# Optimization experiments

Measured on AMD Instinct MI355X. Metric: run time of the kernel, lower is better.

Reference implementation:

```python
import jax, jax.numpy as jnp
import numpy as np

NUM_HEAD = 8
GN_GROUPS = 32
EPS = 1e-5


def group_norm(x, w, b):
    # x: [B,C,H,W]; GroupNorm over 32 groups
    B, C, H, W = x.shape
    xg = x.reshape(B, GN_GROUPS, C // GN_GROUPS, H, W)
    mu = jnp.mean(xg, axis=(2, 3, 4), keepdims=True)
    var = jnp.var(xg, axis=(2, 3, 4), keepdims=True)
    xn = ((xg - mu) * jax.lax.rsqrt(var + EPS)).reshape(B, C, H, W)
    return xn * w[None, :, None, None] + b[None, :, None, None]


def conv1x1(x, w, b):
    # 1x1 conv == channel-wise linear: w [O,C], x [B,C,H,W]
    return jnp.einsum('oc,bchw->bohw', w, x) + b[None, :, None, None]


def setup_inputs() -> dict:
    key = jax.random.key(0)
    ks = jax.random.split(key, 6)
    B, C, H, W = 8, 512, 32, 32
    s = 1.0 / np.sqrt(C)
    return {
        'x': jax.random.normal(ks[0], (B, C, H, W), jnp.float32),
        'gn_w': jnp.ones((C,), jnp.float32),
        'gn_b': jnp.zeros((C,), jnp.float32),
        'wq': jax.random.normal(ks[1], (C, C), jnp.float32) * s,
        'bq': jnp.zeros((C,), jnp.float32),
        'wk': jax.random.normal(ks[2], (C, C), jnp.float32) * s,
        'bk': jnp.zeros((C,), jnp.float32),
        'wv': jax.random.normal(ks[3], (C, C), jnp.float32) * s,
        'bv': jnp.zeros((C,), jnp.float32),
        'wo': jax.random.normal(ks[4], (C, C), jnp.float32) * s,
        'bo': jnp.zeros((C,), jnp.float32),
    }


def reference(x, gn_w, gn_b, wq, bq, wk, bk, wv, bv, wo, bo):
    B, C, H, W = x.shape
    Hn = NUM_HEAD
    d = C // Hn
    N = H * W
    scale = d ** -0.5

    xn = group_norm(x, gn_w, gn_b)
    q = conv1x1(xn, wq, bq).reshape(B, Hn, d, N)  # [B,Hn,d,N]
    k = conv1x1(xn, wk, bk).reshape(B, Hn, d, N)
    v = conv1x1(xn, wv, bv).reshape(B, Hn, d, N)

    # attn[b,h,i,j] = sum_d q[b,h,d,i] * k[b,h,d,j]
    attn = jnp.einsum('bhdi,bhdj->bhij', q, k) * scale
    attn = jax.nn.softmax(attn, axis=-1)
    # out[b,h,d,i] = sum_j attn[b,h,i,j] * v[b,h,d,j]
    out = jnp.einsum('bhij,bhdj->bhdi', attn, v).reshape(B, C, H, W)
    return x + conv1x1(out, wo, bo)
```

## Files before the change

### kernel.cpp

```cpp
#include <hip/hip_runtime.h>
#include <hip/hip_bf16.h>

typedef unsigned short ushort_t;
typedef __bf16 bf16_t;
typedef bf16_t bf16x8 __attribute__((ext_vector_type(8)));
typedef float f32x4 __attribute__((ext_vector_type(4)));
typedef float f32x16 __attribute__((ext_vector_type(16)));

#define CH 512
#define NSP 1024

__device__ __forceinline__ float bf2f(ushort_t u) {
    union { unsigned int i; float f; } t; t.i = ((unsigned int)u) << 16; return t.f;
}
__device__ __forceinline__ ushort_t f2bf(float f) {
    union { float fl; unsigned int i; } t; t.fl = f;
    unsigned int r = t.i + 0x7fffu + ((t.i >> 16) & 1u);
    return (ushort_t)(r >> 16);
}
__device__ __forceinline__ unsigned int pk2(float a, float b) {
    __hip_bfloat162 h = __float22bfloat162_rn(make_float2(a, b));
    union { __hip_bfloat162 h2; unsigned int u; } t; t.h2 = h; return t.u;
}

#if __has_builtin(__builtin_amdgcn_global_load_lds)
#define HAVE_ASYNC_LDS 1
#endif
__device__ __forceinline__ void cp16(const ushort_t* g, ushort_t* l) {
#ifdef HAVE_ASYNC_LDS
    __builtin_amdgcn_global_load_lds((const __attribute__((address_space(1))) unsigned int*)g,
                                     (__attribute__((address_space(3))) unsigned int*)l, 16, 0, 0);
#else
    *(uint4*)l = *(const uint4*)g;
#endif
}

#if __has_builtin(__builtin_amdgcn_exp2f)
#define EXP2(x) __builtin_amdgcn_exp2f(x)
#else
#define EXP2(x) exp2f(x)
#endif

#define QSCALE 0.18033688011112042f

__global__ __launch_bounds__(256) void prep_kernel(const float* __restrict__ x,
                                                   const float* __restrict__ w0, const float* __restrict__ w1,
                                                   const float* __restrict__ w2, const float* __restrict__ w3,
                                                   float2* __restrict__ gstats, ushort_t* __restrict__ wbf) {
    int tid = threadIdx.x;
    if (blockIdx.x >= 256) {
        int idx = (blockIdx.x - 256) * 256 + tid;
        int my = idx >> 16;
        const float* src = (my == 0) ? w0 : (my == 1) ? w1 : (my == 2) ? w2 : w3;
        float4 v = reinterpret_cast<const float4*>(src)[idx & 65535];
        uint2 u = make_uint2(pk2(v.x, v.y), pk2(v.z, v.w));
        reinterpret_cast<uint2*>(wbf + (size_t)my * 262144)[idx & 65535] = u;
        return;
    }
    __shared__ float red[8];
    int bg = blockIdx.x;
    size_t base = (size_t)bg * 16384;
    float s = 0.f, s2 = 0.f;
    const float4* x4 = reinterpret_cast<const float4*>(x + base);
    for (int i = tid; i < 4096; i += 256) {
        float4 v = x4[i];
        s  += v.x + v.y + v.z + v.w;
        s2 += v.x * v.x + v.y * v.y + v.z * v.z + v.w * v.w;
    }
    #pragma unroll
    for (int off = 32; off > 0; off >>= 1) {
        s  += __shfl_down(s, off, 64);
        s2 += __shfl_down(s2, off, 64);
    }
    int wv = tid >> 6;
    if ((tid & 63) == 0) { red[wv] = s; red[4 + wv] = s2; }
    __syncthreads();
    if (tid == 0) {
        float ts  = red[0] + red[1] + red[2] + red[3];
        float ts2 = red[4] + red[5] + red[6] + red[7];
        float mu  = ts * (1.f / 16384.f);
        float var = ts2 * (1.f / 16384.f) - mu * mu;
        gstats[bg] = make_float2(mu, rsqrtf(var + 1e-5f));
    }
}

__global__ __launch_bounds__(256) void gn_apply(const float* __restrict__ x, const float* __restrict__ gw,
                                                const float* __restrict__ gbias, const float2* __restrict__ gstats,
                                                ushort_t* __restrict__ xnt) {
    __shared__ __align__(16) ushort_t lt[16 * 264];
    int nq = blockIdx.x;
    int bg = blockIdx.y;
    int b = bg >> 5, g = bg & 31;
    int tid = threadIdx.x;
    float2 st = gstats[bg];
    float mu = st.x, rstd = st.y;
    const float4* x4 = reinterpret_cast<const float4*>(x + ((size_t)(b * 512 + g * 16) * 1024 + nq * 256));
    #pragma unroll
    for (int rep = 0; rep < 4; rep++) {
        int id = rep * 256 + tid;
        int cc = id >> 6, j = id & 63;
        float ww = gw[g * 16 + cc], bb = gbias[g * 16 + cc];
        float ca = rstd * ww, cb = bb - mu * ca;
        float4 v = x4[cc * 256 + j];
        uint2 u = make_uint2(pk2(v.x * ca + cb, v.y * ca + cb), pk2(v.z * ca + cb, v.w * ca + cb));
        *reinterpret_cast<uint2*>(&lt[cc * 264 + j * 4]) = u;
    }
    __syncthreads();
    int n = tid;
    ushort_t ov[16];
    #pragma unroll
    for (int cc = 0; cc < 16; cc++) ov[cc] = lt[cc * 264 + n];
    ushort_t* dst = xnt + ((size_t)(b * 1024 + nq * 256 + n)) * 512 + g * 16;
    *reinterpret_cast<ushort4*>(dst + 0)  = *reinterpret_cast<ushort4*>(&ov[0]);
    *reinterpret_cast<ushort4*>(dst + 4)  = *reinterpret_cast<ushort4*>(&ov[4]);
    *reinterpret_cast<ushort4*>(dst + 8)  = *reinterpret_cast<ushort4*>(&ov[8]);
    *reinterpret_cast<ushort4*>(dst + 12) = *reinterpret_cast<ushort4*>(&ov[12]);
}

__global__ __launch_bounds__(256) void conv_qkv(const ushort_t* __restrict__ xnt,
                                                const ushort_t* __restrict__ wbf,
                                                const float* __restrict__ bq,
                                                const float* __restrict__ bk,
                                                const float* __restrict__ bv,
                                                ushort_t* __restrict__ qt,
                                                ushort_t* __restrict__ kt,
                                                ushort_t* __restrict__ vt) {
    __shared__ __align__(16) char smem[17408];
    ushort_t* als = (ushort_t*)smem;
    ushort_t* bls = (ushort_t*)(smem + 8192);
    int tid = threadIdx.x;
    int wave = tid >> 6, lane = tid & 63, l15 = lane & 15, quad = lane >> 4;
    int wm = wave >> 1, wn = wave & 1;
    int m0 = blockIdx.x * 128, o0 = blockIdx.y * 64, b = blockIdx.z;
    const ushort_t* A = xnt + (size_t)b * 524288;

    f32x4 acc[4][2];
    #pragma unroll
    for (int ms = 0; ms < 4; ms++)
        #pragma unroll
        for (int ns = 0; ns < 2; ns++) acc[ms][ns] = (f32x4){0.f, 0.f, 0.f, 0.f};

    for (int k0 = 0; k0 < 512; k0 += 32) {
        #pragma unroll
        for (int rep = 0; rep < 2; rep++) {
            int id = rep * 256 + tid;
            int r = id >> 2, part = id & 3;
            int sw = part ^ ((r >> 2) & 3);
            cp16(A + (size_t)(m0 + r) * 512 + k0 + sw * 8, als + (size_t)id * 8);
        }
        {
            int r = tid >> 2, part = tid & 3;
            int sw = part ^ ((r >> 2) & 3);
            cp16(wbf + (size_t)(o0 + r) * 512 + k0 + sw * 8, bls + (size_t)tid * 8);
        }
        __syncthreads();
        bf16x8 af[4], bfr[2];
        #pragma unroll
        for (int ms = 0; ms < 4; ms++) {
            int row = wm * 64 + ms * 16 + l15;
            int slot = quad ^ ((row >> 2) & 3);
            af[ms] = *(const bf16x8*)(als + row * 32 + slot * 8);
        }
        #pragma unroll
        for (int ns = 0; ns < 2; ns++) {
            int row = wn * 32 + ns * 16 + l15;
            int slot = quad ^ ((row >> 2) & 3);
            bfr[ns] = *(const bf16x8*)(bls + row * 32 + slot * 8);
        }
        #pragma unroll
        for (int ms = 0; ms < 4; ms++)
            #pragma unroll
            for (int ns = 0; ns < 2; ns++)
                acc[ms][ns] = __builtin_amdgcn_mfma_f32_16x16x32_bf16(af[ms], bfr[ns], acc[ms][ns], 0, 0, 0);
        __syncthreads();
    }

    int seg = o0 >> 9, lo = o0 & 511;
    if (seg < 2) {
        const float* bias = seg ? bk : bq;
        ushort_t* dst = seg ? kt : qt;
        float s = seg ? 1.f : QSCALE;
        float bv0 = bias[lo + wn * 32 + l15];
        float bv1 = bias[lo + wn * 32 + 16 + l15];
        ushort_t* cls = (ushort_t*)smem;
        #pragma unroll
        for (int ms = 0; ms < 4; ms++)
            #pragma unroll
            for (int ns = 0; ns < 2; ns++) {
                float bb = ns ? bv1 : bv0;
                int idx = (wm * 64 + ms * 16 + quad * 4) * 64 + wn * 32 + ns * 16 + l15;
                unsigned int ua = pk2((acc[ms][ns][0] + bb) * s, (acc[ms][ns][1] + bb) * s);
                unsigned int ub = pk2((acc[ms][ns][2] + bb) * s, (acc[ms][ns][3] + bb) * s);
                cls[idx]       = (ushort_t)(ua & 0xffff);
                cls[idx + 64]  = (ushort_t)(ua >> 16);
                cls[idx + 128] = (ushort_t)(ub & 0xffff);
                cls[idx + 192] = (ushort_t)(ub >> 16);
            }
        __syncthreads();
        int h = lo >> 6;
        size_t obase = ((size_t)(b * 8 + h) * 1024 + m0) * 64;
        #pragma unroll
        for (int rep = 0; rep < 4; rep++) {
            int id = rep * 256 + tid;
            int r = id >> 3, part = id & 7;
            *(uint4*)(dst + obase + (size_t)r * 64 + part * 8) = *(const uint4*)(cls + r * 64 + part * 8);
        }
    } else {
        float bv0 = bv[lo + wn * 32 + l15];
        float bv1 = bv[lo + wn * 32 + 16 + l15];
        ushort_t* clst = (ushort_t*)smem;
        #pragma unroll
        for (int ms = 0; ms < 4; ms++)
            #pragma unroll
            for (int ns = 0; ns < 2; ns++) {
                float bb = ns ? bv1 : bv0;
                unsigned int ua = pk2(acc[ms][ns][0] + bb, acc[ms][ns][1] + bb);
                unsigned int ub = pk2(acc[ms][ns][2] + bb, acc[ms][ns][3] + bb);
                *(uint2*)(&clst[(wn * 32 + ns * 16 + l15) * 136 + wm * 64 + ms * 16 + quad * 4]) =
                    make_uint2(ua, ub);
            }
        __syncthreads();
        #pragma unroll
        for (int rep = 0; rep < 4; rep++) {
            int id = rep * 256 + tid;
            int row = id >> 4, part = id & 15;
            *(uint4*)(vt + ((size_t)(b * 512 + lo + row) * 1024 + m0 + part * 8)) =
                *(const uint4*)(clst + row * 136 + part * 8);
        }
    }
}

#define Z16 {0.f,0.f,0.f,0.f,0.f,0.f,0.f,0.f,0.f,0.f,0.f,0.f,0.f,0.f,0.f,0.f}

#define PV_STEP(JS, P) {                                                                     \
    unsigned wA0 = pk2(P[((JS)&1)*8+0], P[((JS)&1)*8+1]);                                    \
    unsigned wA1 = pk2(P[((JS)&1)*8+2], P[((JS)&1)*8+3]);                                    \
    unsigned wB0 = pk2(P[((JS)&1)*8+4], P[((JS)&1)*8+5]);                                    \
    unsigned wB1 = pk2(P[((JS)&1)*8+6], P[((JS)&1)*8+7]);                                    \
    asm("v_permlane32_swap_b32 %0, %1" : "+v"(wA0), "+v"(wB0));                              \
    asm("v_permlane32_swap_b32 %0, %1" : "+v"(wA1), "+v"(wB1));                              \
    union { unsigned u[4]; bf16x8 v; } pa_;                                                  \
    pa_.u[0] = wA0; pa_.u[1] = wA1; pa_.u[2] = wB0; pa_.u[3] = wB1;                          \
    int phys_ = (((JS) * 2) | hi) ^ r7;                                                      \
    bf16x8 vf0 = *(const bf16x8*)(vbuf + l31 * 64 + phys_ * 8);                              \
    bf16x8 vf1 = *(const bf16x8*)(vbuf + (32 + l31) * 64 + phys_ * 8);                       \
    __builtin_amdgcn_s_setprio(1);                                                           \
    vacc0 = __builtin_amdgcn_mfma_f32_32x32x16_bf16(pa_.v, vf0, vacc0, 0, 0, 0);             \
    vacc1 = __builtin_amdgcn_mfma_f32_32x32x16_bf16(pa_.v, vf1, vacc1, 0, 0, 0);             \
    __builtin_amdgcn_s_setprio(0); }

__global__ __launch_bounds__(256) void attn_kernel(const ushort_t* __restrict__ qt,
                                                   const ushort_t* __restrict__ kt,
                                                   const ushort_t* __restrict__ vt,
                                                   ushort_t* __restrict__ ao) {
    __shared__ __align__(16) ushort_t smem[16384];
    int tid = threadIdx.x;
    int wave = tid >> 6, lane = tid & 63, l31 = lane & 31, hi = lane >> 5;
    int id = blockIdx.x;
    int bh = (id & 7) * 8 + (id >> 6);
    int i0 = ((id >> 3) & 7) * 128;
    const ushort_t* qb = qt + (size_t)bh * 65536;
    const ushort_t* kb = kt + (size_t)bh * 65536;
    const ushort_t* vb = vt + (size_t)bh * 65536;
    int iw0 = i0 + wave * 32;
    int r7 = l31 & 7;

    bf16x8 qf[4];
    #pragma unroll
    for (int ks = 0; ks < 4; ks++)
        qf[ks] = *(const bf16x8*)(qb + (size_t)(iw0 + l31) * 64 + ks * 16 + hi * 8);

    f32x16 vacc0 = Z16, vacc1 = Z16;
    float lacc = 0.f;

    int rk0 = tid >> 3, sk = tid & 7, rk1 = rk0 + 32;
    const ushort_t* kg0 = kb + rk0 * 64 + (sk ^ (rk0 & 7)) * 8;
    const ushort_t* kg1 = kb + rk1 * 64 + (sk ^ (rk1 & 7)) * 8;
    const ushort_t* vg0 = vb + (size_t)rk0 * 1024 + (sk ^ (rk0 & 7)) * 8;
    const ushort_t* vg1 = vb + (size_t)rk1 * 1024 + (sk ^ (rk1 & 7)) * 8;

    cp16(kg0, smem + tid * 8);
    cp16(kg1, smem + (tid + 256) * 8);
    cp16(vg0, smem + 8192 + tid * 8);
    cp16(vg1, smem + 8192 + (tid + 256) * 8);
    kg0 += 4096; kg1 += 4096; vg0 += 64; vg1 += 64;
    __syncthreads();

    for (int jt = 0; jt < 16; jt++) {
        int cur = jt & 1;
        if (jt < 15) {
            ushort_t* kd = smem + (cur ^ 1) * 4096;
            ushort_t* vd = smem + 8192 + (cur ^ 1) * 4096;
            cp16(kg0, kd + tid * 8);
            cp16(kg1, kd + (tid + 256) * 8);
            cp16(vg0, vd + tid * 8);
            cp16(vg1, vd + (tid + 256) * 8);
            kg0 += 4096; kg1 += 4096; vg0 += 64; vg1 += 64;
        }
        const ushort_t* kbuf = smem + cur * 4096;
        const ushort_t* vbuf = smem + 8192 + cur * 4096;

        f32x16 s0 = Z16, s1 = Z16;
        __builtin_amdgcn_s_setprio(1);
        #pragma unroll
        for (int ks = 0; ks < 4; ks++) {
            int phys = ((ks * 2) | hi) ^ r7;
            bf16x8 kf = *(const bf16x8*)(kbuf + l31 * 64 + phys * 8);
            s0 = __builtin_amdgcn_mfma_f32_32x32x16_bf16(kf, qf[ks], s0, 0, 0, 0);
        }
        #pragma unroll
        for (int ks = 0; ks < 4; ks++) {
            int phys = ((ks * 2) | hi) ^ r7;
            bf16x8 kf = *(const bf16x8*)(kbuf + (32 + l31) * 64 + phys * 8);
            s1 = __builtin_amdgcn_mfma_f32_32x32x16_bf16(kf, qf[ks], s1, 0, 0, 0);
        }
        __builtin_amdgcn_s_setprio(0);

        float p0[16], p1[16];
        #pragma unroll
        for (int r = 0; r < 16; r++) p0[r] = EXP2(s0[r]);
        #pragma unroll
        for (int r = 0; r < 16; r++) p1[r] = EXP2(s1[r]);
        float t0 = 0.f, t1 = 0.f, t2 = 0.f, t3 = 0.f;
        #pragma unroll
        for (int r = 0; r < 4; r++) { t0 += p0[r]; t1 += p0[4 + r]; t2 += p0[8 + r]; t3 += p0[12 + r]; }
        #pragma unroll
        for (int r = 0; r < 4; r++) { t0 += p1[r]; t1 += p1[4 + r]; t2 += p1[8 + r]; t3 += p1[12 + r]; }
        lacc += (t0 + t1) + (t2 + t3);

        PV_STEP(0, p0)
        PV_STEP(1, p0)
        PV_STEP(2, p1)
        PV_STEP(3, p1)

        __syncthreads();
    }

    lacc += __shfl_xor(lacc, 32, 64);
    float linv[16];
    #pragma unroll
    for (int r = 0; r < 16; r++) {
        int ir = (r & 3) + 8 * (r >> 2) + 4 * hi;
        linv[r] = 1.f / __shfl(lacc, ir, 64);
    }

    ushort_t* ols = smem;
    #pragma unroll
    for (int r = 0; r < 16; r++) {
        int irow = wave * 32 + (r & 3) + 8 * (r >> 2) + 4 * hi;
        ols[irow * 80 + l31]      = f2bf(vacc0[r] * linv[r]);
        ols[irow * 80 + 32 + l31] = f2bf(vacc1[r] * linv[r]);
    }
    __syncthreads();
    int b = bh >> 3, h = bh & 7;
    ushort_t* aob = ao + ((size_t)b * 1024 + i0) * 512 + h * 64;
    #pragma unroll
    for (int rep = 0; rep < 4; rep++) {
        int idd = rep * 256 + tid;
        int rl = idd >> 3, part = idd & 7;
        *(uint4*)(aob + (size_t)rl * 512 + part * 8) = *(const uint4*)(ols + rl * 80 + part * 8);
    }
}

__global__ __launch_bounds__(256) void conv_out(const ushort_t* __restrict__ ao,
                                                const ushort_t* __restrict__ wo,
                                                const float* __restrict__ bo,
                                                const float* __restrict__ xres,
                                                float* __restrict__ out) {
    __shared__ __align__(16) char smem[17408];
    ushort_t* als = (ushort_t*)smem;
    ushort_t* bls = (ushort_t*)(smem + 4096);
    int tid = threadIdx.x;
    int wave = tid >> 6, lane = tid & 63, l15 = lane & 15, quad = lane >> 4;
    int wm = wave >> 1, wn = wave & 1;
    int m0 = blockIdx.x * 64, n0 = blockIdx.y * 64, b = blockIdx.z;
    const ushort_t* B = ao + (size_t)b * 524288;

    f32x4 acc[2][2];
    #pragma unroll
    for (int ms = 0; ms < 2; ms++)
        #pragma unroll
        for (int ns = 0; ns < 2; ns++) acc[ms][ns] = (f32x4){0.f, 0.f, 0.f, 0.f};

    for (int k0 = 0; k0 < 512; k0 += 32) {
        {
            int r = tid >> 2, part = tid & 3;
            int sw = part ^ ((r >> 2) & 3);
            cp16(wo + (size_t)(m0 + r) * 512 + k0 + sw * 8, als + (size_t)tid * 8);
            cp16(B + (size_t)(n0 + r) * 512 + k0 + sw * 8, bls + (size_t)tid * 8);
        }
        __syncthreads();
        bf16x8 af[2], bfr[2];
        #pragma unroll
        for (int ms = 0; ms < 2; ms++) {
            int row = wm * 32 + ms * 16 + l15;
            int slot = quad ^ ((row >> 2) & 3);
            af[ms] = *(const bf16x8*)(als + row * 32 + slot * 8);
        }
        #pragma unroll
        for (int ns = 0; ns < 2; ns++) {
            int row = wn * 32 + ns * 16 + l15;
            int slot = quad ^ ((row >> 2) & 3);
            bfr[ns] = *(const bf16x8*)(bls + row * 32 + slot * 8);
        }
        #pragma unroll
        for (int ms = 0; ms < 2; ms++)
            #pragma unroll
            for (int ns = 0; ns < 2; ns++)
                acc[ms][ns] = __builtin_amdgcn_mfma_f32_16x16x32_bf16(af[ms], bfr[ns], acc[ms][ns], 0, 0, 0);
        __syncthreads();
    }

    float* clsf = (float*)smem;
    #pragma unroll
    for (int ms = 0; ms < 2; ms++)
        #pragma unroll
        for (int ns = 0; ns < 2; ns++)
            #pragma unroll
            for (int r = 0; r < 4; r++)
                clsf[(wm * 32 + ms * 16 + quad * 4 + r) * 68 + wn * 32 + ns * 16 + l15] = acc[ms][ns][r];
    __syncthreads();
    #pragma unroll
    for (int rep = 0; rep < 4; rep++) {
        int id = rep * 256 + tid;
        int row = id >> 4, part = id & 15;
        float bvr = bo[m0 + row];
        float4 c4 = *(const float4*)(clsf + row * 68 + part * 4);
        size_t ga = ((size_t)(b * 512 + m0 + row)) * 1024 + n0 + part * 4;
        float4 xv = *(const float4*)(xres + ga);
        c4.x += bvr + xv.x; c4.y += bvr + xv.y; c4.z += bvr + xv.z; c4.w += bvr + xv.w;
        *(float4*)(out + ga) = c4;
    }
}

extern "C" void kernel_launch(void* const* d_in, const int* in_sizes, int n_in,
                              void* d_out, int out_size, void* d_ws, size_t ws_size,
                              hipStream_t stream) {
    const float* x    = (const float*)d_in[0];
    const float* gn_w = (const float*)d_in[1];
    const float* gn_b = (const float*)d_in[2];
    const float* wq   = (const float*)d_in[3];
    const float* bq   = (const float*)d_in[4];
    const float* wk   = (const float*)d_in[5];
    const float* bk   = (const float*)d_in[6];
    const float* wv   = (const float*)d_in[7];
    const float* bv   = (const float*)d_in[8];
    const float* wo   = (const float*)d_in[9];
    const float* bo   = (const float*)d_in[10];

    char* ws = (char*)d_ws;
    ushort_t* xnt  = (ushort_t*)(ws);
    ushort_t* qt   = (ushort_t*)(ws + (((size_t)8)  << 20));
    ushort_t* kt   = (ushort_t*)(ws + (((size_t)16) << 20));
    ushort_t* vt   = (ushort_t*)(ws + (((size_t)24) << 20));
    ushort_t* wbf  = (ushort_t*)(ws + (((size_t)32) << 20));
    float2*   gst  = (float2*)  (ws + (((size_t)34) << 20));
    ushort_t* ao   = xnt;

    prep_kernel<<<1280, 256, 0, stream>>>(x, wq, wk, wv, wo, gst, wbf);
    gn_apply<<<dim3(4, 256), 256, 0, stream>>>(x, gn_w, gn_b, gst, xnt);

    conv_qkv<<<dim3(8, 24, 8), 256, 0, stream>>>(xnt, wbf, bq, bk, bv, qt, kt, vt);

    attn_kernel<<<512, 256, 0, stream>>>(qt, kt, vt, ao);

    conv_out<<<dim3(8, 16, 8), 256, 0, stream>>>(ao, wbf + 786432, bo, x, (float*)d_out);
}
```

Before: 167.1 us.

## Split attention blocks to 128 threads and interleave QK/PV per key half

The attention kernel now launches 1024 blocks of 2 waves, each covering 64 query rows instead of 128, so there are more blocks to spread across CUs, with launch bounds requesting two blocks per CU. The K/V tile loads are redistributed over 128 threads using four copies each. The inner loop now computes scores, exp and PV for one 32-key half before starting the next, which shortens live ranges (p0/p1 are no longer held together) and lowers register pressure. In exchange each K/V tile is loaded into shared memory by twice as many blocks, doubling K/V traffic per query row.

```diff
diff --git a/kernel.cpp b/kernel.cpp
--- a/kernel.cpp
+++ b/kernel.cpp
@@ -233,10 +233,10 @@
 #define Z16 {0.f,0.f,0.f,0.f,0.f,0.f,0.f,0.f,0.f,0.f,0.f,0.f,0.f,0.f,0.f,0.f}
 
 #define PV_STEP(JS, P) {                                                                     \
-    unsigned wA0 = pk2(P[((JS)&1)*8+0], P[((JS)&1)*8+1]);                                    \
-    unsigned wA1 = pk2(P[((JS)&1)*8+2], P[((JS)&1)*8+3]);                                    \
-    unsigned wB0 = pk2(P[((JS)&1)*8+4], P[((JS)&1)*8+5]);                                    \
-    unsigned wB1 = pk2(P[((JS)&1)*8+6], P[((JS)&1)*8+7]);                                    \
+    unsigned wA0 = pk2(P[0], P[1]);                                                          \
+    unsigned wA1 = pk2(P[2], P[3]);                                                          \
+    unsigned wB0 = pk2(P[4], P[5]);                                                          \
+    unsigned wB1 = pk2(P[6], P[7]);                                                          \
     asm("v_permlane32_swap_b32 %0, %1" : "+v"(wA0), "+v"(wB0));                              \
     asm("v_permlane32_swap_b32 %0, %1" : "+v"(wA1), "+v"(wB1));                              \
     union { unsigned u[4]; bf16x8 v; } pa_;                                                  \
@@ -249,16 +249,16 @@
     vacc1 = __builtin_amdgcn_mfma_f32_32x32x16_bf16(pa_.v, vf1, vacc1, 0, 0, 0);             \
     __builtin_amdgcn_s_setprio(0); }
 
-__global__ __launch_bounds__(256) void attn_kernel(const ushort_t* __restrict__ qt,
-                                                   const ushort_t* __restrict__ kt,
-                                                   const ushort_t* __restrict__ vt,
-                                                   ushort_t* __restrict__ ao) {
+__global__ __launch_bounds__(128, 2) void attn_kernel(const ushort_t* __restrict__ qt,
+                                                      const ushort_t* __restrict__ kt,
+                                                      const ushort_t* __restrict__ vt,
+                                                      ushort_t* __restrict__ ao) {
     __shared__ __align__(16) ushort_t smem[16384];
     int tid = threadIdx.x;
     int wave = tid >> 6, lane = tid & 63, l31 = lane & 31, hi = lane >> 5;
     int id = blockIdx.x;
-    int bh = (id & 7) * 8 + (id >> 6);
-    int i0 = ((id >> 3) & 7) * 128;
+    int bh = (id & 7) * 8 + (id >> 7);
+    int i0 = ((id >> 3) & 15) * 64;
     const ushort_t* qb = qt + (size_t)bh * 65536;
     const ushort_t* kb = kt + (size_t)bh * 65536;
     const ushort_t* vb = vt + (size_t)bh * 65536;
@@ -273,17 +273,23 @@
     f32x16 vacc0 = Z16, vacc1 = Z16;
     float lacc = 0.f;
 
-    int rk0 = tid >> 3, sk = tid & 7, rk1 = rk0 + 32;
-    const ushort_t* kg0 = kb + rk0 * 64 + (sk ^ (rk0 & 7)) * 8;
-    const ushort_t* kg1 = kb + rk1 * 64 + (sk ^ (rk1 & 7)) * 8;
-    const ushort_t* vg0 = vb + (size_t)rk0 * 1024 + (sk ^ (rk0 & 7)) * 8;
-    const ushort_t* vg1 = vb + (size_t)rk1 * 1024 + (sk ^ (rk1 & 7)) * 8;
-
-    cp16(kg0, smem + tid * 8);
-    cp16(kg1, smem + (tid + 256) * 8);
-    cp16(vg0, smem + 8192 + tid * 8);
-    cp16(vg1, smem + 8192 + (tid + 256) * 8);
-    kg0 += 4096; kg1 += 4096; vg0 += 64; vg1 += 64;
+    int rk = tid >> 3, sk = tid & 7;
+    const ushort_t *kg0, *kg1, *kg2, *kg3, *vg0, *vg1, *vg2, *vg3;
+    {
+        int r0 = rk, r1 = 16 + rk, r2 = 32 + rk, r3 = 48 + rk;
+        int so = (sk ^ (rk & 7)) * 8;
+        kg0 = kb + r0 * 64 + so; kg1 = kb + r1 * 64 + so;
+        kg2 = kb + r2 * 64 + so; kg3 = kb + r3 * 64 + so;
+        vg0 = vb + (size_t)r0 * 1024 + so; vg1 = vb + (size_t)r1 * 1024 + so;
+        vg2 = vb + (size_t)r2 * 1024 + so; vg3 = vb + (size_t)r3 * 1024 + so;
+    }
+
+    cp16(kg0, smem + tid * 8);            cp16(kg1, smem + 1024 + tid * 8);
+    cp16(kg2, smem + 2048 + tid * 8);     cp16(kg3, smem + 3072 + tid * 8);
+    cp16(vg0, smem + 8192 + tid * 8);     cp16(vg1, smem + 9216 + tid * 8);
+    cp16(vg2, smem + 10240 + tid * 8);    cp16(vg3, smem + 11264 + tid * 8);
+    kg0 += 4096; kg1 += 4096; kg2 += 4096; kg3 += 4096;
+    vg0 += 64; vg1 += 64; vg2 += 64; vg3 += 64;
     __syncthreads();
 
     for (int jt = 0; jt < 16; jt++) {
@@ -291,47 +297,56 @@
         if (jt < 15) {
             ushort_t* kd = smem + (cur ^ 1) * 4096;
             ushort_t* vd = smem + 8192 + (cur ^ 1) * 4096;
-            cp16(kg0, kd + tid * 8);
-            cp16(kg1, kd + (tid + 256) * 8);
-            cp16(vg0, vd + tid * 8);
-            cp16(vg1, vd + (tid + 256) * 8);
-            kg0 += 4096; kg1 += 4096; vg0 += 64; vg1 += 64;
+            cp16(kg0, kd + tid * 8);           cp16(kg1, kd + 1024 + tid * 8);
+            cp16(kg2, kd + 2048 + tid * 8);    cp16(kg3, kd + 3072 + tid * 8);
+            cp16(vg0, vd + tid * 8);           cp16(vg1, vd + 1024 + tid * 8);
+            cp16(vg2, vd + 2048 + tid * 8);    cp16(vg3, vd + 3072 + tid * 8);
+            kg0 += 4096; kg1 += 4096; kg2 += 4096; kg3 += 4096;
+            vg0 += 64; vg1 += 64; vg2 += 64; vg3 += 64;
         }
         const ushort_t* kbuf = smem + cur * 4096;
         const ushort_t* vbuf = smem + 8192 + cur * 4096;
 
-        f32x16 s0 = Z16, s1 = Z16;
-        __builtin_amdgcn_s_setprio(1);
-        #pragma unroll
-        for (int ks = 0; ks < 4; ks++) {
-            int phys = ((ks * 2) | hi) ^ r7;
-            bf16x8 kf = *(const bf16x8*)(kbuf + l31 * 64 + phys * 8);
-            s0 = __builtin_amdgcn_mfma_f32_32x32x16_bf16(kf, qf[ks], s0, 0, 0, 0);
-        }
-        #pragma unroll
-        for (int ks = 0; ks < 4; ks++) {
-            int phys = ((ks * 2) | hi) ^ r7;
-            bf16x8 kf = *(const bf16x8*)(kbuf + (32 + l31) * 64 + phys * 8);
-            s1 = __builtin_amdgcn_mfma_f32_32x32x16_bf16(kf, qf[ks], s1, 0, 0, 0);
-        }
-        __builtin_amdgcn_s_setprio(0);
-
-        float p0[16], p1[16];
-        #pragma unroll
-        for (int r = 0; r < 16; r++) p0[r] = EXP2(s0[r]);
-        #pragma unroll
-        for (int r = 0; r < 16; r++) p1[r] = EXP2(s1[r]);
-        float t0 = 0.f, t1 = 0.f, t2 = 0.f, t3 = 0.f;
-        #pragma unroll
-        for (int r = 0; r < 4; r++) { t0 += p0[r]; t1 += p0[4 + r]; t2 += p0[8 + r]; t3 += p0[12 + r]; }
-        #pragma unroll
-        for (int r = 0; r < 4; r++) { t0 += p1[r]; t1 += p1[4 + r]; t2 += p1[8 + r]; t3 += p1[12 + r]; }
-        lacc += (t0 + t1) + (t2 + t3);
-
-        PV_STEP(0, p0)
-        PV_STEP(1, p0)
-        PV_STEP(2, p1)
-        PV_STEP(3, p1)
+        {
+            f32x16 s0 = Z16;
+            __builtin_amdgcn_s_setprio(1);
+            #pragma unroll
+            for (int ks = 0; ks < 4; ks++) {
+                int phys = ((ks * 2) | hi) ^ r7;
+                bf16x8 kf = *(const bf16x8*)(kbuf + l31 * 64 + phys * 8);
+                s0 = __builtin_amdgcn_mfma_f32_32x32x16_bf16(kf, qf[ks], s0, 0, 0, 0);
+            }
+            __builtin_amdgcn_s_setprio(0);
+            float p0[16];
+            #pragma unroll
+            for (int r = 0; r < 16; r++) p0[r] = EXP2(s0[r]);
+            float t0 = 0.f, t1 = 0.f, t2 = 0.f, t3 = 0.f;
+            #pragma unroll
+            for (int r = 0; r < 4; r++) { t0 += p0[r]; t1 += p0[4 + r]; t2 += p0[8 + r]; t3 += p0[12 + r]; }
+            lacc += (t0 + t1) + (t2 + t3);
+            PV_STEP(0, (p0))
+            PV_STEP(1, (p0 + 8))
+        }
+        {
+            f32x16 s1 = Z16;
+            __builtin_amdgcn_s_setprio(1);
+            #pragma unroll
+            for (int ks = 0; ks < 4; ks++) {
+                int phys = ((ks * 2) | hi) ^ r7;
+                bf16x8 kf = *(const bf16x8*)(kbuf + (32 + l31) * 64 + phys * 8);
+                s1 = __builtin_amdgcn_mfma_f32_32x32x16_bf16(kf, qf[ks], s1, 0, 0, 0);
+            }
+            __builtin_amdgcn_s_setprio(0);
+            float p1[16];
+            #pragma unroll
+            for (int r = 0; r < 16; r++) p1[r] = EXP2(s1[r]);
+            float t0 = 0.f, t1 = 0.f, t2 = 0.f, t3 = 0.f;
+            #pragma unroll
+            for (int r = 0; r < 4; r++) { t0 += p1[r]; t1 += p1[4 + r]; t2 += p1[8 + r]; t3 += p1[12 + r]; }
+            lacc += (t0 + t1) + (t2 + t3);
+            PV_STEP(2, (p1))
+            PV_STEP(3, (p1 + 8))
+        }
 
         __syncthreads();
     }
@@ -356,7 +371,7 @@
     ushort_t* aob = ao + ((size_t)b * 1024 + i0) * 512 + h * 64;
     #pragma unroll
     for (int rep = 0; rep < 4; rep++) {
-        int idd = rep * 256 + tid;
+        int idd = rep * 128 + tid;
         int rl = idd >> 3, part = idd & 7;
         *(uint4*)(aob + (size_t)rl * 512 + part * 8) = *(const uint4*)(ols + rl * 80 + part * 8);
     }
@@ -462,7 +477,7 @@
 
     conv_qkv<<<dim3(8, 24, 8), 256, 0, stream>>>(xnt, wbf, bq, bk, bv, qt, kt, vt);
 
-    attn_kernel<<<512, 256, 0, stream>>>(qt, kt, vt, ao);
+    attn_kernel<<<1024, 128, 0, stream>>>(qt, kt, vt, ao);
 
     conv_out<<<dim3(8, 16, 8), 256, 0, stream>>>(ao, wbf + 786432, bo, x, (float*)d_out);
 }
```

Measured after the change: 170.3 us. About the same (+2.0%).

## Enlarge GEMM tiles to 128x128 in QKV and output 1x1 convolutions

Applied to the files above, without the earlier changes.

Both projection GEMMs now use 128x128 output tiles with a 4x4 MFMA accumulator grid per wave, which raises arithmetic intensity and halves or quarters the number of blocks. The output conv swaps operand roles so activations are the M side, and its epilogue writes straight from registers with fused bias and residual add, dropping the LDS transpose. The V path also writes directly from registers, while the Q/K path stages two heads through LDS in turn. The cost is higher register pressure and fewer blocks, e.g. 256 for conv_out, which may underfill the GPU, plus narrower, less coalesced 8-byte and 16-byte global stores.

```diff
diff --git a/kernel.cpp b/kernel.cpp
--- a/kernel.cpp
+++ b/kernel.cpp
@@ -125,20 +125,20 @@
                                                 ushort_t* __restrict__ qt,
                                                 ushort_t* __restrict__ kt,
                                                 ushort_t* __restrict__ vt) {
-    __shared__ __align__(16) char smem[17408];
+    __shared__ __align__(16) char smem[16384];
     ushort_t* als = (ushort_t*)smem;
     ushort_t* bls = (ushort_t*)(smem + 8192);
     int tid = threadIdx.x;
     int wave = tid >> 6, lane = tid & 63, l15 = lane & 15, quad = lane >> 4;
     int wm = wave >> 1, wn = wave & 1;
-    int m0 = blockIdx.x * 128, o0 = blockIdx.y * 64, b = blockIdx.z;
+    int m0 = blockIdx.x * 128, o0 = blockIdx.y * 128, b = blockIdx.z;
     const ushort_t* A = xnt + (size_t)b * 524288;
 
-    f32x4 acc[4][2];
+    f32x4 acc[4][4];
     #pragma unroll
     for (int ms = 0; ms < 4; ms++)
         #pragma unroll
-        for (int ns = 0; ns < 2; ns++) acc[ms][ns] = (f32x4){0.f, 0.f, 0.f, 0.f};
+        for (int ns = 0; ns < 4; ns++) acc[ms][ns] = (f32x4){0.f, 0.f, 0.f, 0.f};
 
     for (int k0 = 0; k0 < 512; k0 += 32) {
         #pragma unroll
@@ -147,14 +147,10 @@
             int r = id >> 2, part = id & 3;
             int sw = part ^ ((r >> 2) & 3);
             cp16(A + (size_t)(m0 + r) * 512 + k0 + sw * 8, als + (size_t)id * 8);
-        }
-        {
-            int r = tid >> 2, part = tid & 3;
-            int sw = part ^ ((r >> 2) & 3);
-            cp16(wbf + (size_t)(o0 + r) * 512 + k0 + sw * 8, bls + (size_t)tid * 8);
+            cp16(wbf + (size_t)(o0 + r) * 512 + k0 + sw * 8, bls + (size_t)id * 8);
         }
         __syncthreads();
-        bf16x8 af[4], bfr[2];
+        bf16x8 af[4], bfr[4];
         #pragma unroll
         for (int ms = 0; ms < 4; ms++) {
             int row = wm * 64 + ms * 16 + l15;
@@ -162,15 +158,15 @@
             af[ms] = *(const bf16x8*)(als + row * 32 + slot * 8);
         }
         #pragma unroll
-        for (int ns = 0; ns < 2; ns++) {
-            int row = wn * 32 + ns * 16 + l15;
+        for (int ns = 0; ns < 4; ns++) {
+            int row = wn * 64 + ns * 16 + l15;
             int slot = quad ^ ((row >> 2) & 3);
             bfr[ns] = *(const bf16x8*)(bls + row * 32 + slot * 8);
         }
         #pragma unroll
         for (int ms = 0; ms < 4; ms++)
             #pragma unroll
-            for (int ns = 0; ns < 2; ns++)
+            for (int ns = 0; ns < 4; ns++)
                 acc[ms][ns] = __builtin_amdgcn_mfma_f32_16x16x32_bf16(af[ms], bfr[ns], acc[ms][ns], 0, 0, 0);
         __syncthreads();
     }
@@ -180,52 +176,48 @@
         const float* bias = seg ? bk : bq;
         ushort_t* dst = seg ? kt : qt;
         float s = seg ? 1.f : QSCALE;
-        float bv0 = bias[lo + wn * 32 + l15];
-        float bv1 = bias[lo + wn * 32 + 16 + l15];
         ushort_t* cls = (ushort_t*)smem;
         #pragma unroll
-        for (int ms = 0; ms < 4; ms++)
+        for (int oh = 0; oh < 2; oh++) {
+            if (oh) __syncthreads();
+            if (wn == oh) {
+                #pragma unroll
+                for (int ns = 0; ns < 4; ns++) {
+                    float bb = bias[lo + oh * 64 + ns * 16 + l15];
+                    #pragma unroll
+                    for (int ms = 0; ms < 4; ms++) {
+                        int idx = (wm * 64 + ms * 16 + quad * 4) * 64 + ns * 16 + l15;
+                        unsigned ua = pk2((acc[ms][ns][0] + bb) * s, (acc[ms][ns][1] + bb) * s);
+                        unsigned ub = pk2((acc[ms][ns][2] + bb) * s, (acc[ms][ns][3] + bb) * s);
+                        cls[idx]       = (ushort_t)(ua & 0xffff);
+                        cls[idx + 64]  = (ushort_t)(ua >> 16);
+                        cls[idx + 128] = (ushort_t)(ub & 0xffff);
+                        cls[idx + 192] = (ushort_t)(ub >> 16);
+                    }
+                }
+            }
+            __syncthreads();
+            int h = (lo >> 6) + oh;
+            size_t obase = ((size_t)(b * 8 + h) * 1024 + m0) * 64;
             #pragma unroll
-            for (int ns = 0; ns < 2; ns++) {
-                float bb = ns ? bv1 : bv0;
-                int idx = (wm * 64 + ms * 16 + quad * 4) * 64 + wn * 32 + ns * 16 + l15;
-                unsigned int ua = pk2((acc[ms][ns][0] + bb) * s, (acc[ms][ns][1] + bb) * s);
-                unsigned int ub = pk2((acc[ms][ns][2] + bb) * s, (acc[ms][ns][3] + bb) * s);
-                cls[idx]       = (ushort_t)(ua & 0xffff);
-                cls[idx + 64]  = (ushort_t)(ua >> 16);
-                cls[idx + 128] = (ushort_t)(ub & 0xffff);
-                cls[idx + 192] = (ushort_t)(ub >> 16);
+            for (int rep = 0; rep < 4; rep++) {
+                int idd = rep * 256 + tid;
+                int r = idd >> 3, part = idd & 7;
+                *(uint4*)(dst + obase + (size_t)r * 64 + part * 8) = *(const uint4*)(cls + r * 64 + part * 8);
             }
-        __syncthreads();
-        int h = lo >> 6;
-        size_t obase = ((size_t)(b * 8 + h) * 1024 + m0) * 64;
-        #pragma unroll
-        for (int rep = 0; rep < 4; rep++) {
-            int id = rep * 256 + tid;
-            int r = id >> 3, part = id & 7;
-            *(uint4*)(dst + obase + (size_t)r * 64 + part * 8) = *(const uint4*)(cls + r * 64 + part * 8);
         }
     } else {
-        float bv0 = bv[lo + wn * 32 + l15];
-        float bv1 = bv[lo + wn * 32 + 16 + l15];
-        ushort_t* clst = (ushort_t*)smem;
-        #pragma unroll
-        for (int ms = 0; ms < 4; ms++)
+        #pragma unroll
+        for (int ns = 0; ns < 4; ns++) {
+            int c = lo + wn * 64 + ns * 16 + l15;
+            float bb = bv[c];
             #pragma unroll
-            for (int ns = 0; ns < 2; ns++) {
-                float bb = ns ? bv1 : bv0;
-                unsigned int ua = pk2(acc[ms][ns][0] + bb, acc[ms][ns][1] + bb);
-                unsigned int ub = pk2(acc[ms][ns][2] + bb, acc[ms][ns][3] + bb);
-                *(uint2*)(&clst[(wn * 32 + ns * 16 + l15) * 136 + wm * 64 + ms * 16 + quad * 4]) =
-                    make_uint2(ua, ub);
+            for (int ms = 0; ms < 4; ms++) {
+                int n = m0 + wm * 64 + ms * 16 + quad * 4;
+                uint2 u = make_uint2(pk2(acc[ms][ns][0] + bb, acc[ms][ns][1] + bb),
+                                     pk2(acc[ms][ns][2] + bb, acc[ms][ns][3] + bb));
+                *(uint2*)(vt + ((size_t)(b * 512 + c)) * 1024 + n) = u;
             }
-        __syncthreads();
-        #pragma unroll
-        for (int rep = 0; rep < 4; rep++) {
-            int id = rep * 256 + tid;
-            int row = id >> 4, part = id & 15;
-            *(uint4*)(vt + ((size_t)(b * 512 + lo + row) * 1024 + m0 + part * 8)) =
-                *(const uint4*)(clst + row * 136 + part * 8);
         }
     }
 }
@@ -367,69 +359,68 @@
                                                 const float* __restrict__ bo,
                                                 const float* __restrict__ xres,
                                                 float* __restrict__ out) {
-    __shared__ __align__(16) char smem[17408];
+    __shared__ __align__(16) char smem[16384];
     ushort_t* als = (ushort_t*)smem;
-    ushort_t* bls = (ushort_t*)(smem + 4096);
+    ushort_t* bls = (ushort_t*)(smem + 8192);
     int tid = threadIdx.x;
     int wave = tid >> 6, lane = tid & 63, l15 = lane & 15, quad = lane >> 4;
     int wm = wave >> 1, wn = wave & 1;
-    int m0 = blockIdx.x * 64, n0 = blockIdx.y * 64, b = blockIdx.z;
-    const ushort_t* B = ao + (size_t)b * 524288;
-
-    f32x4 acc[2][2];
-    #pragma unroll
-    for (int ms = 0; ms < 2; ms++)
-        #pragma unroll
-        for (int ns = 0; ns < 2; ns++) acc[ms][ns] = (f32x4){0.f, 0.f, 0.f, 0.f};
+    int m0 = blockIdx.x * 128, o0 = blockIdx.y * 128, b = blockIdx.z;
+    const ushort_t* A = ao + (size_t)b * 524288;
+
+    f32x4 acc[4][4];
+    #pragma unroll
+    for (int ms = 0; ms < 4; ms++)
+        #pragma unroll
+        for (int ns = 0; ns < 4; ns++) acc[ms][ns] = (f32x4){0.f, 0.f, 0.f, 0.f};
 
     for (int k0 = 0; k0 < 512; k0 += 32) {
-        {
-            int r = tid >> 2, part = tid & 3;
+        #pragma unroll
+        for (int rep = 0; rep < 2; rep++) {
+            int id = rep * 256 + tid;
+            int r = id >> 2, part = id & 3;
             int sw = part ^ ((r >> 2) & 3);
-            cp16(wo + (size_t)(m0 + r) * 512 + k0 + sw * 8, als + (size_t)tid * 8);
-            cp16(B + (size_t)(n0 + r) * 512 + k0 + sw * 8, bls + (size_t)tid * 8);
+            cp16(A + (size_t)(m0 + r) * 512 + k0 + sw * 8, als + (size_t)id * 8);
+            cp16(wo + (size_t)(o0 + r) * 512 + k0 + sw * 8, bls + (size_t)id * 8);
         }
         __syncthreads();
-        bf16x8 af[2], bfr[2];
-        #pragma unroll
-        for (int ms = 0; ms < 2; ms++) {
-            int row = wm * 32 + ms * 16 + l15;
+        bf16x8 af[4], bfr[4];
+        #pragma unroll
+        for (int ms = 0; ms < 4; ms++) {
+            int row = wm * 64 + ms * 16 + l15;
             int slot = quad ^ ((row >> 2) & 3);
             af[ms] = *(const bf16x8*)(als + row * 32 + slot * 8);
         }
         #pragma unroll
-        for (int ns = 0; ns < 2; ns++) {
-            int row = wn * 32 + ns * 16 + l15;
+        for (int ns = 0; ns < 4; ns++) {
+            int row = wn * 64 + ns * 16 + l15;
             int slot = quad ^ ((row >> 2) & 3);
             bfr[ns] = *(const bf16x8*)(bls + row * 32 + slot * 8);
         }
         #pragma unroll
-        for (int ms = 0; ms < 2; ms++)
+        for (int ms = 0; ms < 4; ms++)
             #pragma unroll
-            for (int ns = 0; ns < 2; ns++)
+            for (int ns = 0; ns < 4; ns++)
                 acc[ms][ns] = __builtin_amdgcn_mfma_f32_16x16x32_bf16(af[ms], bfr[ns], acc[ms][ns], 0, 0, 0);
         __syncthreads();
     }
 
-    float* clsf = (float*)smem;
-    #pragma unroll
-    for (int ms = 0; ms < 2; ms++)
-        #pragma unroll
-        for (int ns = 0; ns < 2; ns++)
-            #pragma unroll
-            for (int r = 0; r < 4; r++)
-                clsf[(wm * 32 + ms * 16 + quad * 4 + r) * 68 + wn * 32 + ns * 16 + l15] = acc[ms][ns][r];
-    __syncthreads();
-    #pragma unroll
-    for (int rep = 0; rep < 4; rep++) {
-        int id = rep * 256 + tid;
-        int row = id >> 4, part = id & 15;
-        float bvr = bo[m0 + row];
-        float4 c4 = *(const float4*)(clsf + row * 68 + part * 4);
-        size_t ga = ((size_t)(b * 512 + m0 + row)) * 1024 + n0 + part * 4;
-        float4 xv = *(const float4*)(xres + ga);
-        c4.x += bvr + xv.x; c4.y += bvr + xv.y; c4.z += bvr + xv.z; c4.w += bvr + xv.w;
-        *(float4*)(out + ga) = c4;
+    #pragma unroll
+    for (int ns = 0; ns < 4; ns++) {
+        int o = o0 + wn * 64 + ns * 16 + l15;
+        float bb = bo[o];
+        #pragma unroll
+        for (int ms = 0; ms < 4; ms++) {
+            int n = m0 + wm * 64 + ms * 16 + quad * 4;
+            size_t ga = ((size_t)(b * 512 + o)) * 1024 + n;
+            float4 xv = *(const float4*)(xres + ga);
+            float4 c4;
+            c4.x = acc[ms][ns][0] + bb + xv.x;
+            c4.y = acc[ms][ns][1] + bb + xv.y;
+            c4.z = acc[ms][ns][2] + bb + xv.z;
+            c4.w = acc[ms][ns][3] + bb + xv.w;
+            *(float4*)(out + ga) = c4;
+        }
     }
 }
 
@@ -460,9 +451,9 @@
     prep_kernel<<<1280, 256, 0, stream>>>(x, wq, wk, wv, wo, gst, wbf);
     gn_apply<<<dim3(4, 256), 256, 0, stream>>>(x, gn_w, gn_b, gst, xnt);
 
-    conv_qkv<<<dim3(8, 24, 8), 256, 0, stream>>>(xnt, wbf, bq, bk, bv, qt, kt, vt);
+    conv_qkv<<<dim3(8, 12, 8), 256, 0, stream>>>(xnt, wbf, bq, bk, bv, qt, kt, vt);
 
     attn_kernel<<<512, 256, 0, stream>>>(qt, kt, vt, ao);
 
-    conv_out<<<dim3(8, 16, 8), 256, 0, stream>>>(ao, wbf + 786432, bo, x, (float*)d_out);
-}
+    conv_out<<<dim3(8, 4, 8), 256, 0, stream>>>(ao, wbf + 786432, bo, x, (float*)d_out);
+}
```

Result: slower. 174.4 us (+4.4%).

## Fuse group-norm stats and apply into one kernel; retile output conv

Applied to the files above, without the earlier changes.

Group-norm statistics and normalization now run in one kernel that holds the whole group in registers, which removes the second read of x and the gstats round trip. Weight conversion moves to its own kernel. The output 1x1 conv swaps operand roles so spatial positions form the M tile (128 wide) and output channels the N tile. Results are written straight from MFMA accumulators with the residual add, dropping the LDS staging pass. Risks are higher register pressure in the fused GN kernel, which runs only 256 blocks, and less coalesced epilogue stores.

```diff
diff --git a/kernel.cpp b/kernel.cpp
--- a/kernel.cpp
+++ b/kernel.cpp
@@ -43,29 +43,32 @@
 
 #define QSCALE 0.18033688011112042f
 
-__global__ __launch_bounds__(256) void prep_kernel(const float* __restrict__ x,
-                                                   const float* __restrict__ w0, const float* __restrict__ w1,
-                                                   const float* __restrict__ w2, const float* __restrict__ w3,
-                                                   float2* __restrict__ gstats, ushort_t* __restrict__ wbf) {
-    int tid = threadIdx.x;
-    if (blockIdx.x >= 256) {
-        int idx = (blockIdx.x - 256) * 256 + tid;
-        int my = idx >> 16;
-        const float* src = (my == 0) ? w0 : (my == 1) ? w1 : (my == 2) ? w2 : w3;
-        float4 v = reinterpret_cast<const float4*>(src)[idx & 65535];
-        uint2 u = make_uint2(pk2(v.x, v.y), pk2(v.z, v.w));
-        reinterpret_cast<uint2*>(wbf + (size_t)my * 262144)[idx & 65535] = u;
-        return;
-    }
+__global__ __launch_bounds__(256) void prep_w(const float* __restrict__ w0, const float* __restrict__ w1,
+                                              const float* __restrict__ w2, const float* __restrict__ w3,
+                                              ushort_t* __restrict__ wbf) {
+    int idx = blockIdx.x * 256 + threadIdx.x;
+    int my = idx >> 16;
+    const float* src = (my == 0) ? w0 : (my == 1) ? w1 : (my == 2) ? w2 : w3;
+    float4 v = reinterpret_cast<const float4*>(src)[idx & 65535];
+    uint2 u = make_uint2(pk2(v.x, v.y), pk2(v.z, v.w));
+    reinterpret_cast<uint2*>(wbf + (size_t)my * 262144)[idx & 65535] = u;
+}
+
+__global__ __launch_bounds__(256) void gn_fused(const float* __restrict__ x, const float* __restrict__ gw,
+                                                const float* __restrict__ gbias,
+                                                ushort_t* __restrict__ xnt) {
     __shared__ float red[8];
     int bg = blockIdx.x;
-    size_t base = (size_t)bg * 16384;
+    int b = bg >> 5, g = bg & 31;
+    int tid = threadIdx.x;
+    const float4* x4 = reinterpret_cast<const float4*>(x + (size_t)bg * 16384);
+    float4 v[16];
     float s = 0.f, s2 = 0.f;
-    const float4* x4 = reinterpret_cast<const float4*>(x + base);
-    for (int i = tid; i < 4096; i += 256) {
-        float4 v = x4[i];
-        s  += v.x + v.y + v.z + v.w;
-        s2 += v.x * v.x + v.y * v.y + v.z * v.z + v.w * v.w;
+    #pragma unroll
+    for (int i = 0; i < 16; i++) {
+        v[i] = x4[i * 256 + tid];
+        s  += v[i].x + v[i].y + v[i].z + v[i].w;
+        s2 += v[i].x * v[i].x + v[i].y * v[i].y + v[i].z * v[i].z + v[i].w * v[i].w;
     }
     #pragma unroll
     for (int off = 32; off > 0; off >>= 1) {
@@ -75,46 +78,31 @@
     int wv = tid >> 6;
     if ((tid & 63) == 0) { red[wv] = s; red[4 + wv] = s2; }
     __syncthreads();
-    if (tid == 0) {
-        float ts  = red[0] + red[1] + red[2] + red[3];
-        float ts2 = red[4] + red[5] + red[6] + red[7];
-        float mu  = ts * (1.f / 16384.f);
-        float var = ts2 * (1.f / 16384.f) - mu * mu;
-        gstats[bg] = make_float2(mu, rsqrtf(var + 1e-5f));
-    }
-}
-
-__global__ __launch_bounds__(256) void gn_apply(const float* __restrict__ x, const float* __restrict__ gw,
-                                                const float* __restrict__ gbias, const float2* __restrict__ gstats,
-                                                ushort_t* __restrict__ xnt) {
-    __shared__ __align__(16) ushort_t lt[16 * 264];
-    int nq = blockIdx.x;
-    int bg = blockIdx.y;
-    int b = bg >> 5, g = bg & 31;
-    int tid = threadIdx.x;
-    float2 st = gstats[bg];
-    float mu = st.x, rstd = st.y;
-    const float4* x4 = reinterpret_cast<const float4*>(x + ((size_t)(b * 512 + g * 16) * 1024 + nq * 256));
-    #pragma unroll
-    for (int rep = 0; rep < 4; rep++) {
-        int id = rep * 256 + tid;
-        int cc = id >> 6, j = id & 63;
+    float ts  = red[0] + red[1] + red[2] + red[3];
+    float ts2 = red[4] + red[5] + red[6] + red[7];
+    float mu  = ts * (1.f / 16384.f);
+    float var = ts2 * (1.f / 16384.f) - mu * mu;
+    float rstd = rsqrtf(var + 1e-5f);
+    float ca[16], cb[16];
+    #pragma unroll
+    for (int cc = 0; cc < 16; cc++) {
         float ww = gw[g * 16 + cc], bb = gbias[g * 16 + cc];
-        float ca = rstd * ww, cb = bb - mu * ca;
-        float4 v = x4[cc * 256 + j];
-        uint2 u = make_uint2(pk2(v.x * ca + cb, v.y * ca + cb), pk2(v.z * ca + cb, v.w * ca + cb));
-        *reinterpret_cast<uint2*>(&lt[cc * 264 + j * 4]) = u;
-    }
-    __syncthreads();
-    int n = tid;
-    ushort_t ov[16];
-    #pragma unroll
-    for (int cc = 0; cc < 16; cc++) ov[cc] = lt[cc * 264 + n];
-    ushort_t* dst = xnt + ((size_t)(b * 1024 + nq * 256 + n)) * 512 + g * 16;
-    *reinterpret_cast<ushort4*>(dst + 0)  = *reinterpret_cast<ushort4*>(&ov[0]);
-    *reinterpret_cast<ushort4*>(dst + 4)  = *reinterpret_cast<ushort4*>(&ov[4]);
-    *reinterpret_cast<ushort4*>(dst + 8)  = *reinterpret_cast<ushort4*>(&ov[8]);
-    *reinterpret_cast<ushort4*>(dst + 12) = *reinterpret_cast<ushort4*>(&ov[12]);
+        ca[cc] = rstd * ww; cb[cc] = bb - mu * ca[cc];
+    }
+    #pragma unroll
+    for (int jj = 0; jj < 4; jj++) {
+        float e[16];
+        #pragma unroll
+        for (int cc = 0; cc < 16; cc++) {
+            float xv = (jj == 0) ? v[cc].x : (jj == 1) ? v[cc].y : (jj == 2) ? v[cc].z : v[cc].w;
+            e[cc] = xv * ca[cc] + cb[cc];
+        }
+        uint4 u0 = make_uint4(pk2(e[0], e[1]), pk2(e[2], e[3]), pk2(e[4], e[5]), pk2(e[6], e[7]));
+        uint4 u1 = make_uint4(pk2(e[8], e[9]), pk2(e[10], e[11]), pk2(e[12], e[13]), pk2(e[14], e[15]));
+        ushort_t* dst = xnt + ((size_t)(b * 1024 + 4 * tid + jj)) * 512 + g * 16;
+        *reinterpret_cast<uint4*>(dst)     = u0;
+        *reinterpret_cast<uint4*>(dst + 8) = u1;
+    }
 }
 
 __global__ __launch_bounds__(256) void conv_qkv(const ushort_t* __restrict__ xnt,
@@ -367,33 +355,39 @@
                                                 const float* __restrict__ bo,
                                                 const float* __restrict__ xres,
                                                 float* __restrict__ out) {
-    __shared__ __align__(16) char smem[17408];
+    __shared__ __align__(16) char smem[12288];
     ushort_t* als = (ushort_t*)smem;
-    ushort_t* bls = (ushort_t*)(smem + 4096);
+    ushort_t* bls = (ushort_t*)(smem + 8192);
     int tid = threadIdx.x;
     int wave = tid >> 6, lane = tid & 63, l15 = lane & 15, quad = lane >> 4;
     int wm = wave >> 1, wn = wave & 1;
-    int m0 = blockIdx.x * 64, n0 = blockIdx.y * 64, b = blockIdx.z;
-    const ushort_t* B = ao + (size_t)b * 524288;
-
-    f32x4 acc[2][2];
-    #pragma unroll
-    for (int ms = 0; ms < 2; ms++)
+    int m0 = blockIdx.x * 128, o0 = blockIdx.y * 64, b = blockIdx.z;
+    const ushort_t* A = ao + (size_t)b * 524288;
+
+    f32x4 acc[4][2];
+    #pragma unroll
+    for (int ms = 0; ms < 4; ms++)
         #pragma unroll
         for (int ns = 0; ns < 2; ns++) acc[ms][ns] = (f32x4){0.f, 0.f, 0.f, 0.f};
 
     for (int k0 = 0; k0 < 512; k0 += 32) {
+        #pragma unroll
+        for (int rep = 0; rep < 2; rep++) {
+            int id = rep * 256 + tid;
+            int r = id >> 2, part = id & 3;
+            int sw = part ^ ((r >> 2) & 3);
+            cp16(A + (size_t)(m0 + r) * 512 + k0 + sw * 8, als + (size_t)id * 8);
+        }
         {
             int r = tid >> 2, part = tid & 3;
             int sw = part ^ ((r >> 2) & 3);
-            cp16(wo + (size_t)(m0 + r) * 512 + k0 + sw * 8, als + (size_t)tid * 8);
-            cp16(B + (size_t)(n0 + r) * 512 + k0 + sw * 8, bls + (size_t)tid * 8);
-        }
-        __syncthreads();
-        bf16x8 af[2], bfr[2];
-        #pragma unroll
-        for (int ms = 0; ms < 2; ms++) {
-            int row = wm * 32 + ms * 16 + l15;
+            cp16(wo + (size_t)(o0 + r) * 512 + k0 + sw * 8, bls + (size_t)tid * 8);
+        }
+        __syncthreads();
+        bf16x8 af[4], bfr[2];
+        #pragma unroll
+        for (int ms = 0; ms < 4; ms++) {
+            int row = wm * 64 + ms * 16 + l15;
             int slot = quad ^ ((row >> 2) & 3);
             af[ms] = *(const bf16x8*)(als + row * 32 + slot * 8);
         }
@@ -404,32 +398,29 @@
             bfr[ns] = *(const bf16x8*)(bls + row * 32 + slot * 8);
         }
         #pragma unroll
-        for (int ms = 0; ms < 2; ms++)
+        for (int ms = 0; ms < 4; ms++)
             #pragma unroll
             for (int ns = 0; ns < 2; ns++)
                 acc[ms][ns] = __builtin_amdgcn_mfma_f32_16x16x32_bf16(af[ms], bfr[ns], acc[ms][ns], 0, 0, 0);
         __syncthreads();
     }
 
-    float* clsf = (float*)smem;
-    #pragma unroll
-    for (int ms = 0; ms < 2; ms++)
-        #pragma unroll
-        for (int ns = 0; ns < 2; ns++)
-            #pragma unroll
-            for (int r = 0; r < 4; r++)
-                clsf[(wm * 32 + ms * 16 + quad * 4 + r) * 68 + wn * 32 + ns * 16 + l15] = acc[ms][ns][r];
-    __syncthreads();
-    #pragma unroll
-    for (int rep = 0; rep < 4; rep++) {
-        int id = rep * 256 + tid;
-        int row = id >> 4, part = id & 15;
-        float bvr = bo[m0 + row];
-        float4 c4 = *(const float4*)(clsf + row * 68 + part * 4);
-        size_t ga = ((size_t)(b * 512 + m0 + row)) * 1024 + n0 + part * 4;
-        float4 xv = *(const float4*)(xres + ga);
-        c4.x += bvr + xv.x; c4.y += bvr + xv.y; c4.z += bvr + xv.z; c4.w += bvr + xv.w;
-        *(float4*)(out + ga) = c4;
+    #pragma unroll
+    for (int ns = 0; ns < 2; ns++) {
+        int o = o0 + wn * 32 + ns * 16 + l15;
+        float bb = bo[o];
+        #pragma unroll
+        for (int ms = 0; ms < 4; ms++) {
+            int n = m0 + wm * 64 + ms * 16 + quad * 4;
+            size_t ga = ((size_t)(b * 512 + o)) * 1024 + n;
+            float4 xv = *(const float4*)(xres + ga);
+            float4 c4;
+            c4.x = acc[ms][ns][0] + bb + xv.x;
+            c4.y = acc[ms][ns][1] + bb + xv.y;
+            c4.z = acc[ms][ns][2] + bb + xv.z;
+            c4.w = acc[ms][ns][3] + bb + xv.w;
+            *(float4*)(out + ga) = c4;
+        }
     }
 }
 
@@ -454,15 +445,14 @@
     ushort_t* kt   = (ushort_t*)(ws + (((size_t)16) << 20));
     ushort_t* vt   = (ushort_t*)(ws + (((size_t)24) << 20));
     ushort_t* wbf  = (ushort_t*)(ws + (((size_t)32) << 20));
-    float2*   gst  = (float2*)  (ws + (((size_t)34) << 20));
     ushort_t* ao   = xnt;
 
-    prep_kernel<<<1280, 256, 0, stream>>>(x, wq, wk, wv, wo, gst, wbf);
-    gn_apply<<<dim3(4, 256), 256, 0, stream>>>(x, gn_w, gn_b, gst, xnt);
+    prep_w<<<1024, 256, 0, stream>>>(wq, wk, wv, wo, wbf);
+    gn_fused<<<256, 256, 0, stream>>>(x, gn_w, gn_b, xnt);
 
     conv_qkv<<<dim3(8, 24, 8), 256, 0, stream>>>(xnt, wbf, bq, bk, bv, qt, kt, vt);
 
     attn_kernel<<<512, 256, 0, stream>>>(qt, kt, vt, ao);
 
-    conv_out<<<dim3(8, 16, 8), 256, 0, stream>>>(ao, wbf + 786432, bo, x, (float*)d_out);
-}
+    conv_out<<<dim3(8, 8, 8), 256, 0, stream>>>(ao, wbf + 786432, bo, x, (float*)d_out);
+}
```

New measurement: 159.9 us. 1.04x faster.
